# Performance work log

Hardware: AMD Instinct MI355X
Metric: run time of the kernel (lower is better)

## Reference

```python
import jax, jax.numpy as jnp
import numpy as np

N_ROI = 262144
FEATURE_DIM = 256
HIDDEN_DIM = 64
N_NETWORKS = 128


def setup_inputs() -> dict:
    key = jax.random.key(0)
    ks = jax.random.split(key, 5)
    x = jax.random.normal(ks[0], (N_ROI, FEATURE_DIM), dtype=jnp.float32)
    group = jax.random.randint(ks[1], (N_ROI,), 0, N_NETWORKS, dtype=jnp.int32)
    W1 = jax.random.normal(ks[2], (FEATURE_DIM, HIDDEN_DIM), dtype=jnp.float32) / np.sqrt(FEATURE_DIM)
    b1 = jnp.zeros((HIDDEN_DIM,), dtype=jnp.float32)
    W2 = jax.random.normal(ks[3], (HIDDEN_DIM, 1), dtype=jnp.float32) / np.sqrt(HIDDEN_DIM)
    b2 = jnp.zeros((1,), dtype=jnp.float32)
    return {"x": x, "group": group, "W1": W1, "b1": b1, "W2": W2, "b2": b2}


def reference(x, group, W1, b1, W2, b2):
    # attention MLP score per ROI: Linear -> ReLU -> Linear(->1)
    h = jax.nn.relu(x @ W1 + b1)                       # [N, H]
    score = (h @ W2)[:, 0] + b2[0]                     # [N]
    # numerically-stable segment softmax over each network's ROIs
    seg_max = jax.ops.segment_max(score, group, num_segments=N_NETWORKS)  # [K]
    seg_max = jnp.where(jnp.isfinite(seg_max), seg_max, 0.0)              # empty segments -> 0
    w = jnp.exp(score - seg_max[group])                # [N] unnormalized weights
    denom = jax.ops.segment_sum(w, group, num_segments=N_NETWORKS)        # [K]
    num = jax.ops.segment_sum(w[:, None] * x, group, num_segments=N_NETWORKS)  # [K, D]
    # empty networks produce zeros (matches torch.zeros_like branch)
    return jnp.where(denom[:, None] > 0, num / jnp.maximum(denom, 1e-30)[:, None], 0.0)
```

## Files before the change

### kernel.cpp

```cpp
#include <hip/hip_runtime.h>
#include <hip/hip_bf16.h>

#define N_ROI 262144
#define FDIM  256
#define HDIM  64
#define NNET  128

#define CHUNK  32
#define NCHUNK 16
#define RPB    (CHUNK * NCHUNK)
#define NBLK   (N_ROI / RPB)
#define XPITCH 264

typedef __attribute__((ext_vector_type(8))) __bf16 bf16x8;
typedef __attribute__((ext_vector_type(8))) short short8;
typedef __attribute__((ext_vector_type(4))) float floatx4;

union frag_cast { short8 s; bf16x8 b; };

#define NEG_INF (-__builtin_huge_valf())

__device__ __forceinline__ unsigned fkey(float f) {
  unsigned u = __float_as_uint(f);
  return (u & 0x80000000u) ? ~u : (u | 0x80000000u);
}
__device__ __forceinline__ float fkey_inv(unsigned k) {
  unsigned u = (k & 0x80000000u) ? (k ^ 0x80000000u) : ~k;
  return __uint_as_float(u);
}
__device__ __forceinline__ unsigned short f2bf(float f) {
  unsigned u = __float_as_uint(f);
  u += 0x7FFFu + ((u >> 16) & 1u);
  return (unsigned short)(u >> 16);
}
__device__ __forceinline__ float bf2f(unsigned short h) {
  return __uint_as_float(((unsigned)h) << 16);
}
__device__ __forceinline__ unsigned cvt2(float a, float b) {
  union { __hip_bfloat162 h; unsigned u; } cv;
  cv.h = __float22bfloat162_rn(make_float2(a, b));
  return cv.u;
}
__device__ __forceinline__ int sidx(int row, int s) {
  return row * XPITCH + (s ^ (((row >> 3) & 3) << 4));
}

__global__ __launch_bounds__(256, 2) void fused_kernel(
    const float* __restrict__ x, const int* __restrict__ group,
    const float* __restrict__ W1, const float* __restrict__ b1,
    const float* __restrict__ W2,
    float* __restrict__ num_ws,
    float* __restrict__ m_ws)
{
  __shared__ unsigned short w1t[HDIM][XPITCH];
  __shared__ __align__(16) unsigned short xl[CHUNK * XPITCH];
  __shared__ float scpart[4][CHUNK];
  __shared__ float sc[CHUNK];
  __shared__ int   ggrp[RPB];
  __shared__ unsigned gw[CHUNK];
  __shared__ unsigned tmax[NNET];
  __shared__ __align__(16) float fl[NNET];
  __shared__ float mrun[NNET], dent[NNET], denrun[NNET];

  const int tid  = threadIdx.x;
  const int wave = tid >> 6, lane = tid & 63;
  const int col  = lane & 15, quad = lane >> 4;

  {
    const int n = tid & 63, kg = tid >> 6;
    for (int p = 0; p < 8; ++p) {
      const int k0 = p * 32 + kg * 8;
      unsigned short tmp[8];
#pragma unroll
      for (int j = 0; j < 8; ++j) tmp[j] = f2bf(W1[(k0 + j) * HDIM + n]);
      *(short8*)&w1t[n][k0] = *(short8*)tmp;
    }
  }
  if (tid < NNET) { mrun[tid] = NEG_INF; denrun[tid] = 0.f; }

  const size_t rbase = (size_t)blockIdx.x * RPB;
  ggrp[tid]       = group[rbase + tid];
  ggrp[tid + 256] = group[rbase + tid + 256];

  const float b1s = b1[wave * 16 + col];
  const float w2s = W2[wave * 16 + col];

  floatx4 acc[8][4];
#pragma unroll
  for (int mt = 0; mt < 8; ++mt)
#pragma unroll
    for (int nt = 0; nt < 4; ++nt) acc[mt][nt] = (floatx4)0.f;

  const float* xb = x + rbase * FDIM;

  float4 pf[8];
#pragma unroll
  for (int i = 0; i < 8; ++i)
    pf[i] = *(const float4*)(xb + i * 1024 + tid * 4);

  for (int ch = 0; ch < NCHUNK; ++ch) {
    __syncthreads();
#pragma unroll
    for (int i = 0; i < 8; ++i) {
      const int row = i * 4 + wave;
      uint2 pk; pk.x = cvt2(pf[i].x, pf[i].y); pk.y = cvt2(pf[i].z, pf[i].w);
      *(uint2*)&xl[sidx(row, lane * 4)] = pk;
    }
    if (tid < NNET) tmax[tid] = 0u;
    __syncthreads();

    if (ch < NCHUNK - 1) {
      const float* xn = xb + (size_t)(ch + 1) * CHUNK * FDIM;
#pragma unroll
      for (int i = 0; i < 8; ++i)
        pf[i] = *(const float4*)(xn + i * 1024 + tid * 4);
    }

    floatx4 accS[2];
    accS[0] = (floatx4)0.f; accS[1] = (floatx4)0.f;
#pragma unroll
    for (int c = 0; c < 8; ++c) {
      frag_cast bw;
      bw.s = *(const short8*)&w1t[wave * 16 + col][c * 32 + quad * 8];
#pragma unroll
      for (int mt = 0; mt < 2; ++mt) {
        frag_cast af;
        af.s = *(const short8*)&xl[sidx(mt * 16 + col, c * 32 + quad * 8)];
        accS[mt] = __builtin_amdgcn_mfma_f32_16x16x32_bf16(af.b, bw.b, accS[mt], 0, 0, 0);
      }
    }
#pragma unroll
    for (int mt = 0; mt < 2; ++mt) {
      float pr[4];
#pragma unroll
      for (int r = 0; r < 4; ++r) pr[r] = fmaxf(accS[mt][r] + b1s, 0.f) * w2s;
#pragma unroll
      for (int off = 1; off < 16; off <<= 1)
#pragma unroll
        for (int r = 0; r < 4; ++r) pr[r] += __shfl_xor(pr[r], off, 16);
      if (col == 0) {
#pragma unroll
        for (int r = 0; r < 4; ++r) scpart[wave][mt * 16 + quad * 4 + r] = pr[r];
      }
    }
    __syncthreads();
    if (tid < CHUNK) {
      const float s = scpart[0][tid] + scpart[1][tid] + scpart[2][tid] + scpart[3][tid];
      sc[tid] = s;
      atomicMax(&tmax[ggrp[ch * CHUNK + tid]], fkey(s));
    }
    __syncthreads();
    if (tid < NNET) {
      const unsigned tk = tmax[tid];
      float f = 1.f;
      if (tk) {
        const float mo = mrun[tid];
        const float mn = fmaxf(mo, fkey_inv(tk));
        f = __expf(mo - mn);
        mrun[tid] = mn;
      }
      fl[tid] = f;
      dent[tid] = 0.f;
    }
    __syncthreads();
    if (tid < CHUNK) {
      const int g = ggrp[ch * CHUNK + tid];
      const float w = __expf(sc[tid] - mrun[g]);
      const unsigned short wb = f2bf(w);
      gw[tid] = ((unsigned)g << 16) | wb;
      atomicAdd(&dent[g], bf2f(wb));
    }
#pragma unroll
    for (int mt = 0; mt < 8; ++mt) {
      const floatx4 f4 = *(const floatx4*)&fl[mt * 16 + quad * 4];
#pragma unroll
      for (int nt = 0; nt < 4; ++nt)
#pragma unroll
        for (int r = 0; r < 4; ++r) acc[mt][nt][r] *= f4[r];
    }
    __syncthreads();

    unsigned gwv[8];
#pragma unroll
    for (int j = 0; j < 8; ++j) gwv[j] = gw[quad * 8 + j];
    frag_cast bfx[4];
#pragma unroll
    for (int nt = 0; nt < 4; ++nt) {
      unsigned short bb[8];
#pragma unroll
      for (int j = 0; j < 8; ++j)
        bb[j] = xl[sidx(quad * 8 + j, wave * 64 + nt * 16 + col)];
      bfx[nt].s = *(short8*)bb;
    }
#pragma unroll
    for (int mt = 0; mt < 8; ++mt) {
      const unsigned gt = (unsigned)(mt * 16 + col);
      unsigned short aa[8];
#pragma unroll
      for (int j = 0; j < 8; ++j)
        aa[j] = ((gwv[j] >> 16) == gt) ? (unsigned short)gwv[j] : (unsigned short)0;
      frag_cast af; af.s = *(short8*)aa;
#pragma unroll
      for (int nt = 0; nt < 4; ++nt)
        acc[mt][nt] = __builtin_amdgcn_mfma_f32_16x16x32_bf16(af.b, bfx[nt].b, acc[mt][nt], 0, 0, 0);
    }
    if (tid < NNET) denrun[tid] = denrun[tid] * fl[tid] + dent[tid];
  }

  float* slice = num_ws + (size_t)blockIdx.x * (NNET * 257);
#pragma unroll
  for (int mt = 0; mt < 8; ++mt)
#pragma unroll
    for (int nt = 0; nt < 4; ++nt)
#pragma unroll
      for (int r = 0; r < 4; ++r)
        slice[(mt * 16 + quad * 4 + r) * 257 + wave * 64 + nt * 16 + col] = acc[mt][nt][r];
  if (tid < NNET) {
    slice[tid * 257 + 256] = denrun[tid];
    m_ws[(size_t)blockIdx.x * NNET + tid] = mrun[tid];
  }
}

__global__ __launch_bounds__(256) void finalize_kernel(
    const float* __restrict__ num_ws, const float* __restrict__ m_ws,
    float* __restrict__ out)
{
  const int g     = blockIdx.x >> 1;
  const int dbase = (blockIdx.x & 1) << 7;
  const int tid   = threadIdx.x;
  __shared__ float e_l[NBLK];
  __shared__ float red[8];
  __shared__ float npart[2][128];

  const float m0 = m_ws[(size_t)tid * NNET + g];
  const float m1 = m_ws[(size_t)(tid + 256) * NNET + g];
  float M = fmaxf(m0, m1);
#pragma unroll
  for (int off = 1; off < 64; off <<= 1) M = fmaxf(M, __shfl_xor(M, off));
  if ((tid & 63) == 0) red[tid >> 6] = M;
  __syncthreads();
  M = fmaxf(fmaxf(red[0], red[1]), fmaxf(red[2], red[3]));

  const float e0 = (m0 == NEG_INF) ? 0.f : __expf(m0 - M);
  const float e1 = (m1 == NEG_INF) ? 0.f : __expf(m1 - M);
  e_l[tid]       = e0;
  e_l[tid + 256] = e1;
  float dp = num_ws[(size_t)tid * (NNET * 257) + g * 257 + 256] * e0
           + num_ws[(size_t)(tid + 256) * (NNET * 257) + g * 257 + 256] * e1;
#pragma unroll
  for (int off = 1; off < 64; off <<= 1) dp += __shfl_xor(dp, off);
  if ((tid & 63) == 0) red[4 + (tid >> 6)] = dp;
  __syncthreads();
  const float den = red[4] + red[5] + red[6] + red[7];

  const int dd = tid & 127, half = tid >> 7;
  float nsum = 0.f;
  const float* base = num_ws + (size_t)half * 256 * (NNET * 257) + g * 257 + dbase + dd;
  const float* el   = e_l + half * 256;
#pragma unroll 4
  for (int b = 0; b < 256; ++b)
    nsum += base[(size_t)b * (NNET * 257)] * el[b];
  npart[half][dd] = nsum;
  __syncthreads();
  if (tid < 128) {
    const float num = npart[0][tid] + npart[1][tid];
    out[g * FDIM + dbase + tid] = (den > 0.f) ? num / fmaxf(den, 1e-30f) : 0.f;
  }
}

extern "C" void kernel_launch(void* const* d_in, const int* in_sizes, int n_in,
                              void* d_out, int out_size, void* d_ws, size_t ws_size,
                              hipStream_t stream)
{
  const float* x     = (const float*)d_in[0];
  const int*   group = (const int*)d_in[1];
  const float* W1    = (const float*)d_in[2];
  const float* b1    = (const float*)d_in[3];
  const float* W2    = (const float*)d_in[4];
  float* out = (float*)d_out;

  float* num_ws = (float*)d_ws;
  float* m_ws   = num_ws + (size_t)NBLK * NNET * 257;

  fused_kernel<<<NBLK, 256, 0, stream>>>(x, group, W1, b1, W2, num_ws, m_ws);
  finalize_kernel<<<2 * NNET, 256, 0, stream>>>(num_ws, m_ws, out);

  (void)in_sizes; (void)n_in; (void)out_size; (void)ws_size;
}
```

Baseline: 429.0 us.

## Double-buffer x tiles, keep W1 in registers, restructure softmax bookkeeping and workspace layout

The main kernel now double-buffers the bf16 x tile and a per-network weight matrix in LDS, which removes several block-wide barriers per chunk. W1 fragments are held in registers instead of being staged through LDS. The per-chunk max, rescale and weight computation is handled by one wave using register state. The one-hot A operand is built in an LDS matrix rather than by per-lane compares. The workspace is transposed to a group-major layout so the finalize kernel uses one 512-thread block per network and reads contiguously. The trade-off is more LDS (two x buffers plus zero-filled A matrices), wave-0 serialization on the softmax step, and extra per-chunk zeroing of the A buffer.

Measured after the change: 520.0 us. +21.2%, slower.

```diff
diff --git a/kernel.cpp b/kernel.cpp
--- a/kernel.cpp
+++ b/kernel.cpp
@@ -11,6 +11,7 @@
 #define RPB    (CHUNK * NCHUNK)
 #define NBLK   (N_ROI / RPB)
 #define XPITCH 264
+#define APITCH 40
 
 typedef __attribute__((ext_vector_type(8))) __bf16 bf16x8;
 typedef __attribute__((ext_vector_type(8))) short short8;
@@ -50,38 +51,32 @@
     const float* __restrict__ W1, const float* __restrict__ b1,
     const float* __restrict__ W2,
     float* __restrict__ num_ws,
+    float* __restrict__ den_ws,
     float* __restrict__ m_ws)
 {
-  __shared__ unsigned short w1t[HDIM][XPITCH];
-  __shared__ __align__(16) unsigned short xl[CHUNK * XPITCH];
+  __shared__ __align__(16) unsigned short xl[2][CHUNK * XPITCH];
+  __shared__ __align__(16) unsigned short Alds[2][NNET * APITCH];
   __shared__ float scpart[4][CHUNK];
-  __shared__ float sc[CHUNK];
-  __shared__ int   ggrp[RPB];
-  __shared__ unsigned gw[CHUNK];
   __shared__ unsigned tmax[NNET];
   __shared__ __align__(16) float fl[NNET];
-  __shared__ float mrun[NNET], dent[NNET], denrun[NNET];
+  __shared__ float mrunL[NNET];
+  __shared__ float dentf[NNET];
 
   const int tid  = threadIdx.x;
   const int wave = tid >> 6, lane = tid & 63;
   const int col  = lane & 15, quad = lane >> 4;
-
-  {
-    const int n = tid & 63, kg = tid >> 6;
-    for (int p = 0; p < 8; ++p) {
-      const int k0 = p * 32 + kg * 8;
-      unsigned short tmp[8];
-#pragma unroll
-      for (int j = 0; j < 8; ++j) tmp[j] = f2bf(W1[(k0 + j) * HDIM + n]);
-      *(short8*)&w1t[n][k0] = *(short8*)tmp;
-    }
-  }
-  if (tid < NNET) { mrun[tid] = NEG_INF; denrun[tid] = 0.f; }
-
-  const size_t rbase = (size_t)blockIdx.x * RPB;
-  ggrp[tid]       = group[rbase + tid];
-  ggrp[tid + 256] = group[rbase + tid + 256];
-
+  const int bid  = blockIdx.x;
+  const size_t rbase = (size_t)bid * RPB;
+
+  frag_cast w1f[8];
+#pragma unroll
+  for (int c = 0; c < 8; ++c) {
+    unsigned short tmp[8];
+#pragma unroll
+    for (int j = 0; j < 8; ++j)
+      tmp[j] = f2bf(W1[(c * 32 + quad * 8 + j) * HDIM + wave * 16 + col]);
+    w1f[c].s = *(short8*)tmp;
+  }
   const float b1s = b1[wave * 16 + col];
   const float w2s = W2[wave * 16 + col];
 
@@ -91,42 +86,47 @@
 #pragma unroll
     for (int nt = 0; nt < 4; ++nt) acc[mt][nt] = (floatx4)0.f;
 
+  float mreg[2] = {NEG_INF, NEG_INF};
+  float dreg[2] = {0.f, 0.f};
+
   const float* xb = x + rbase * FDIM;
-
   float4 pf[8];
 #pragma unroll
   for (int i = 0; i < 8; ++i)
     pf[i] = *(const float4*)(xb + i * 1024 + tid * 4);
 
+  const short8 zero8 = (short8)0;
+
+#pragma unroll
+  for (int i = 0; i < 8; ++i) {
+    const int row = i * 4 + wave;
+    uint2 pk; pk.x = cvt2(pf[i].x, pf[i].y); pk.y = cvt2(pf[i].z, pf[i].w);
+    *(uint2*)&xl[0][sidx(row, (tid & 63) * 4)] = pk;
+  }
+  for (int k8 = tid; k8 < (NNET * APITCH) / 8; k8 += 256)
+    *(short8*)&Alds[0][k8 * 8] = zero8;
+  __syncthreads();
+
   for (int ch = 0; ch < NCHUNK; ++ch) {
-    __syncthreads();
-#pragma unroll
-    for (int i = 0; i < 8; ++i) {
-      const int row = i * 4 + wave;
-      uint2 pk; pk.x = cvt2(pf[i].x, pf[i].y); pk.y = cvt2(pf[i].z, pf[i].w);
-      *(uint2*)&xl[sidx(row, lane * 4)] = pk;
-    }
-    if (tid < NNET) tmax[tid] = 0u;
-    __syncthreads();
-
+    const int b = ch & 1;
+
+    int gch = 0;
+    if (wave == 0) gch = group[rbase + ch * 32 + (lane & 31)];
     if (ch < NCHUNK - 1) {
-      const float* xn = xb + (size_t)(ch + 1) * CHUNK * FDIM;
 #pragma unroll
       for (int i = 0; i < 8; ++i)
-        pf[i] = *(const float4*)(xn + i * 1024 + tid * 4);
+        pf[i] = *(const float4*)(xb + (ch + 1) * 8192 + i * 1024 + tid * 4);
     }
 
     floatx4 accS[2];
     accS[0] = (floatx4)0.f; accS[1] = (floatx4)0.f;
 #pragma unroll
     for (int c = 0; c < 8; ++c) {
-      frag_cast bw;
-      bw.s = *(const short8*)&w1t[wave * 16 + col][c * 32 + quad * 8];
 #pragma unroll
       for (int mt = 0; mt < 2; ++mt) {
         frag_cast af;
-        af.s = *(const short8*)&xl[sidx(mt * 16 + col, c * 32 + quad * 8)];
-        accS[mt] = __builtin_amdgcn_mfma_f32_16x16x32_bf16(af.b, bw.b, accS[mt], 0, 0, 0);
+        af.s = *(const short8*)&xl[b][sidx(mt * 16 + col, c * 32 + quad * 8)];
+        accS[mt] = __builtin_amdgcn_mfma_f32_16x16x32_bf16(af.b, w1f[c].b, accS[mt], 0, 0, 0);
       }
     }
 #pragma unroll
@@ -144,32 +144,50 @@
       }
     }
     __syncthreads();
-    if (tid < CHUNK) {
-      const float s = scpart[0][tid] + scpart[1][tid] + scpart[2][tid] + scpart[3][tid];
-      sc[tid] = s;
-      atomicMax(&tmax[ggrp[ch * CHUNK + tid]], fkey(s));
+
+    if (wave == 0) {
+      tmax[lane] = 0u; tmax[lane + 64] = 0u;
+      dentf[lane] = 0.f; dentf[lane + 64] = 0.f;
+      const int l = lane & 31;
+      const float s = scpart[0][l] + scpart[1][l] + scpart[2][l] + scpart[3][l];
+      asm volatile("s_waitcnt lgkmcnt(0)" ::: "memory");
+      if (lane < 32) atomicMax(&tmax[gch], fkey(s));
+      asm volatile("s_waitcnt lgkmcnt(0)" ::: "memory");
+#pragma unroll
+      for (int h = 0; h < 2; ++h) {
+        const int gi = lane + h * 64;
+        const unsigned tk = tmax[gi];
+        float f = 1.f;
+        if (tk) {
+          const float mn = fmaxf(mreg[h], fkey_inv(tk));
+          f = __expf(mreg[h] - mn);
+          mreg[h] = mn;
+        }
+        fl[gi] = f; mrunL[gi] = mreg[h]; dreg[h] *= f;
+      }
+      asm volatile("s_waitcnt lgkmcnt(0)" ::: "memory");
+      if (lane < 32) {
+        const float w = __expf(s - mrunL[gch]);
+        const unsigned short wb = f2bf(w);
+        Alds[b][gch * APITCH + lane] = wb;
+        atomicAdd(&dentf[gch], bf2f(wb));
+      }
+      asm volatile("s_waitcnt lgkmcnt(0)" ::: "memory");
+      dreg[0] += dentf[lane];
+      dreg[1] += dentf[lane + 64];
+    }
+    if (ch < NCHUNK - 1) {
+#pragma unroll
+      for (int i = 0; i < 8; ++i) {
+        const int row = i * 4 + wave;
+        uint2 pk; pk.x = cvt2(pf[i].x, pf[i].y); pk.y = cvt2(pf[i].z, pf[i].w);
+        *(uint2*)&xl[b ^ 1][sidx(row, (tid & 63) * 4)] = pk;
+      }
+      for (int k8 = tid; k8 < (NNET * APITCH) / 8; k8 += 256)
+        *(short8*)&Alds[b ^ 1][k8 * 8] = zero8;
     }
     __syncthreads();
-    if (tid < NNET) {
-      const unsigned tk = tmax[tid];
-      float f = 1.f;
-      if (tk) {
-        const float mo = mrun[tid];
-        const float mn = fmaxf(mo, fkey_inv(tk));
-        f = __expf(mo - mn);
-        mrun[tid] = mn;
-      }
-      fl[tid] = f;
-      dent[tid] = 0.f;
-    }
-    __syncthreads();
-    if (tid < CHUNK) {
-      const int g = ggrp[ch * CHUNK + tid];
-      const float w = __expf(sc[tid] - mrun[g]);
-      const unsigned short wb = f2bf(w);
-      gw[tid] = ((unsigned)g << 16) | wb;
-      atomicAdd(&dent[g], bf2f(wb));
-    }
+
 #pragma unroll
     for (int mt = 0; mt < 8; ++mt) {
       const floatx4 f4 = *(const floatx4*)&fl[mt * 16 + quad * 4];
@@ -178,93 +196,86 @@
 #pragma unroll
         for (int r = 0; r < 4; ++r) acc[mt][nt][r] *= f4[r];
     }
-    __syncthreads();
-
-    unsigned gwv[8];
-#pragma unroll
-    for (int j = 0; j < 8; ++j) gwv[j] = gw[quad * 8 + j];
     frag_cast bfx[4];
 #pragma unroll
     for (int nt = 0; nt < 4; ++nt) {
       unsigned short bb[8];
 #pragma unroll
       for (int j = 0; j < 8; ++j)
-        bb[j] = xl[sidx(quad * 8 + j, wave * 64 + nt * 16 + col)];
+        bb[j] = xl[b][sidx(quad * 8 + j, wave * 64 + nt * 16 + col)];
       bfx[nt].s = *(short8*)bb;
     }
 #pragma unroll
     for (int mt = 0; mt < 8; ++mt) {
-      const unsigned gt = (unsigned)(mt * 16 + col);
-      unsigned short aa[8];
-#pragma unroll
-      for (int j = 0; j < 8; ++j)
-        aa[j] = ((gwv[j] >> 16) == gt) ? (unsigned short)gwv[j] : (unsigned short)0;
-      frag_cast af; af.s = *(short8*)aa;
+      frag_cast af;
+      af.s = *(const short8*)&Alds[b][(mt * 16 + col) * APITCH + quad * 8];
 #pragma unroll
       for (int nt = 0; nt < 4; ++nt)
         acc[mt][nt] = __builtin_amdgcn_mfma_f32_16x16x32_bf16(af.b, bfx[nt].b, acc[mt][nt], 0, 0, 0);
     }
-    if (tid < NNET) denrun[tid] = denrun[tid] * fl[tid] + dent[tid];
-  }
-
-  float* slice = num_ws + (size_t)blockIdx.x * (NNET * 257);
+  }
+
 #pragma unroll
   for (int mt = 0; mt < 8; ++mt)
 #pragma unroll
-    for (int nt = 0; nt < 4; ++nt)
-#pragma unroll
-      for (int r = 0; r < 4; ++r)
-        slice[(mt * 16 + quad * 4 + r) * 257 + wave * 64 + nt * 16 + col] = acc[mt][nt][r];
-  if (tid < NNET) {
-    slice[tid * 257 + 256] = denrun[tid];
-    m_ws[(size_t)blockIdx.x * NNET + tid] = mrun[tid];
-  }
-}
-
-__global__ __launch_bounds__(256) void finalize_kernel(
-    const float* __restrict__ num_ws, const float* __restrict__ m_ws,
-    float* __restrict__ out)
+    for (int r = 0; r < 4; ++r) {
+      const int g = mt * 16 + quad * 4 + r;
+      float* rp = num_ws + ((size_t)g * NBLK + bid) * FDIM;
+#pragma unroll
+      for (int nt = 0; nt < 4; ++nt)
+        rp[wave * 64 + nt * 16 + col] = acc[mt][nt][r];
+    }
+  if (wave == 0) {
+    den_ws[(size_t)lane * NBLK + bid]        = dreg[0];
+    den_ws[(size_t)(lane + 64) * NBLK + bid] = dreg[1];
+    m_ws[(size_t)lane * NBLK + bid]          = mreg[0];
+    m_ws[(size_t)(lane + 64) * NBLK + bid]   = mreg[1];
+  }
+}
+
+__global__ __launch_bounds__(512) void finalize_kernel(
+    const float* __restrict__ num_ws, const float* __restrict__ den_ws,
+    const float* __restrict__ m_ws, float* __restrict__ out)
 {
-  const int g     = blockIdx.x >> 1;
-  const int dbase = (blockIdx.x & 1) << 7;
-  const int tid   = threadIdx.x;
+  const int g   = blockIdx.x;
+  const int tid = threadIdx.x;
   __shared__ float e_l[NBLK];
-  __shared__ float red[8];
-  __shared__ float npart[2][128];
-
-  const float m0 = m_ws[(size_t)tid * NNET + g];
-  const float m1 = m_ws[(size_t)(tid + 256) * NNET + g];
-  float M = fmaxf(m0, m1);
+  __shared__ float red[16];
+  __shared__ float npart[2][FDIM];
+
+  const float mb = m_ws[(size_t)g * NBLK + tid];
+  float M = mb;
 #pragma unroll
   for (int off = 1; off < 64; off <<= 1) M = fmaxf(M, __shfl_xor(M, off));
   if ((tid & 63) == 0) red[tid >> 6] = M;
   __syncthreads();
-  M = fmaxf(fmaxf(red[0], red[1]), fmaxf(red[2], red[3]));
-
-  const float e0 = (m0 == NEG_INF) ? 0.f : __expf(m0 - M);
-  const float e1 = (m1 == NEG_INF) ? 0.f : __expf(m1 - M);
-  e_l[tid]       = e0;
-  e_l[tid + 256] = e1;
-  float dp = num_ws[(size_t)tid * (NNET * 257) + g * 257 + 256] * e0
-           + num_ws[(size_t)(tid + 256) * (NNET * 257) + g * 257 + 256] * e1;
+  M = red[0];
+#pragma unroll
+  for (int wv = 1; wv < 8; ++wv) M = fmaxf(M, red[wv]);
+
+  const float eb = (mb == NEG_INF) ? 0.f : __expf(mb - M);
+  e_l[tid] = eb;
+  float dp = den_ws[(size_t)g * NBLK + tid] * eb;
 #pragma unroll
   for (int off = 1; off < 64; off <<= 1) dp += __shfl_xor(dp, off);
-  if ((tid & 63) == 0) red[4 + (tid >> 6)] = dp;
+  if ((tid & 63) == 0) red[8 + (tid >> 6)] = dp;
   __syncthreads();
-  const float den = red[4] + red[5] + red[6] + red[7];
-
-  const int dd = tid & 127, half = tid >> 7;
+  float den = red[8];
+#pragma unroll
+  for (int wv = 1; wv < 8; ++wv) den += red[8 + wv];
+
+  const int d = tid & 255, half = tid >> 8;
+  const float* base = num_ws + ((size_t)g * NBLK + half * 256) * FDIM + d;
+  const float* el   = e_l + half * 256;
   float nsum = 0.f;
-  const float* base = num_ws + (size_t)half * 256 * (NNET * 257) + g * 257 + dbase + dd;
-  const float* el   = e_l + half * 256;
-#pragma unroll 4
+#pragma unroll 8
   for (int b = 0; b < 256; ++b)
-    nsum += base[(size_t)b * (NNET * 257)] * el[b];
-  npart[half][dd] = nsum;
+    nsum += base[(size_t)b * FDIM] * el[b];
+  npart[half][d] = nsum;
   __syncthreads();
-  if (tid < 128) {
+  if (tid < FDIM) {
     const float num = npart[0][tid] + npart[1][tid];
-    out[g * FDIM + dbase + tid] = (den > 0.f) ? num / fmaxf(den, 1e-30f) : 0.f;
+    out[g * FDIM + tid] = (den > 0.f) ? num / fmaxf(den, 1e-30f) : 0.f;
   }
 }
 
@@ -280,10 +291,11 @@
   float* out = (float*)d_out;
 
   float* num_ws = (float*)d_ws;
-  float* m_ws   = num_ws + (size_t)NBLK * NNET * 257;
-
-  fused_kernel<<<NBLK, 256, 0, stream>>>(x, group, W1, b1, W2, num_ws, m_ws);
-  finalize_kernel<<<2 * NNET, 256, 0, stream>>>(num_ws, m_ws, out);
+  float* den_ws = num_ws + (size_t)NNET * NBLK * FDIM;
+  float* m_ws   = den_ws + (size_t)NNET * NBLK;
+
+  fused_kernel<<<NBLK, 256, 0, stream>>>(x, group, W1, b1, W2, num_ws, den_ws, m_ws);
+  finalize_kernel<<<NNET, 512, 0, stream>>>(num_ws, den_ws, m_ws, out);
 
   (void)in_sizes; (void)n_in; (void)out_size; (void)ws_size;
 }
```
